# Optimization experiments

Measured on AMD Instinct MI355X. Metric: run time of the kernel, lower is better.

Reference implementation:

```python
import jax, jax.numpy as jnp
import numpy as np

B, T, C = 2, 2048, 2048
H, HD = 16, 128          # n_head, head_dim
DC, DC1 = 672, 672        # kv / q compression dims
DR = 64                   # decoupled rope dim
DN = HD - DR              # nope dim = 64
GATE_CH = 32


def _rope(x, cos, sin):
    # x: (B,T,h,D); cos/sin: (B,T,D//2) -> broadcast over heads
    cos = cos[:, :, None, :]
    sin = sin[:, :, None, :]
    d = x.shape[-1] // 2
    x1, x2 = x[..., :d], x[..., d:]
    return jnp.concatenate([x1 * cos + x2 * sin, -x1 * sin + x2 * cos], axis=-1)


def _rmsnorm(x):
    eps = jnp.finfo(x.dtype).eps
    return x * jax.lax.rsqrt(jnp.mean(jnp.square(x), axis=-1, keepdims=True) + eps)


def setup_inputs() -> dict:
    key = jax.random.key(0)
    ks = jax.random.split(key, 10)
    x = jax.random.normal(ks[0], (B, T, C), jnp.float32)
    ve = jax.random.normal(ks[1], (B, T, H * HD), jnp.float32)
    # rotary tables for d_rope//2 = 32 frequencies
    inv_freq = 1.0 / (10000.0 ** (jnp.arange(DR // 2, dtype=jnp.float32) / (DR // 2)))
    ang = jnp.arange(T, dtype=jnp.float32)[:, None] * inv_freq[None, :]  # (T, DR//2)
    cos = jnp.broadcast_to(jnp.cos(ang)[None], (B, T, DR // 2)).astype(jnp.float32)
    sin = jnp.broadcast_to(jnp.sin(ang)[None], (B, T, DR // 2)).astype(jnp.float32)
    s = 0.02
    w_dkv = s * jax.random.normal(ks[2], (C, DC), jnp.float32)
    w_ukv = s * jax.random.normal(ks[3], (DC, H * (DN + HD)), jnp.float32)
    w_kr = s * jax.random.normal(ks[4], (C, DR), jnp.float32)
    w_dq = s * jax.random.normal(ks[5], (C, DC1), jnp.float32)
    w_q = s * jax.random.normal(ks[6], (DC1, H * HD), jnp.float32)
    w_cproj = s * jax.random.normal(ks[7], (H * HD, C), jnp.float32)
    w_ve_gate = s * jax.random.normal(ks[8], (GATE_CH, H), jnp.float32)
    return {"x": x, "ve": ve, "cos": cos, "sin": sin,
            "w_dkv": w_dkv, "w_ukv": w_ukv, "w_kr": w_kr, "w_dq": w_dq,
            "w_q": w_q, "w_cproj": w_cproj, "w_ve_gate": w_ve_gate,
            "window_size": 0}


def reference(x, ve, cos, sin, w_dkv, w_ukv, w_kr, w_dq, w_q, w_cproj, w_ve_gate, window_size):
    b, t, _ = x.shape
    # low-rank KV path
    c_kv = x @ w_dkv                                   # (B,T,DC)
    kv = (c_kv @ w_ukv).reshape(b, t, H, DN + HD)
    k_nope, v = kv[..., :DN], kv[..., DN:]
    # decoupled rope key (single shared head)
    k_rope = (x @ w_kr).reshape(b, t, 1, DR)
    k_rope = _rope(k_rope, cos, sin)
    # value-embedding gate
    gate = 2.0 * jax.nn.sigmoid(x[..., :GATE_CH] @ w_ve_gate)   # (B,T,H)
    v = v + gate[..., None] * ve.reshape(b, t, H, HD)
    # low-rank Q path
    q = ((x @ w_dq) @ w_q).reshape(b, t, H, HD)
    q_nope, q_rope = q[..., :DN], q[..., DN:]
    q_rope = _rope(q_rope, cos, sin)
    k = jnp.concatenate([k_nope, jnp.broadcast_to(k_rope, (b, t, H, DR))], axis=-1)
    q = jnp.concatenate([q_nope, q_rope], axis=-1)
    q, k = _rmsnorm(q), _rmsnorm(k)
    # causal attention (window_size==0 -> full causal, matching window_size=(-1,-1))
    scale = 1.0 / jnp.sqrt(jnp.float32(HD))
    scores = jnp.einsum('bqhd,bkhd->bhqk', q, k) * scale
    causal = jnp.tril(jnp.ones((t, t), dtype=bool))
    scores = jnp.where(causal[None, None], scores, jnp.finfo(scores.dtype).min)
    att = jax.nn.softmax(scores, axis=-1)
    y = jnp.einsum('bhqk,bkhd->bqhd', att, v).reshape(b, t, H * HD)
    return y @ w_cproj
```

## Files before the change

### kernel.cpp

```cpp
#include <hip/hip_runtime.h>
#include <hip/hip_bf16.h>

typedef unsigned short u16;
typedef unsigned int u32;
typedef __bf16 bf16x8 __attribute__((ext_vector_type(8)));
typedef float f32x4 __attribute__((ext_vector_type(4)));
typedef u16 ushort8 __attribute__((ext_vector_type(8)));

#define TSEQ 2048
#define NHEAD 16

#define GLD16(gp, lp) __builtin_amdgcn_global_load_lds( \
    (__attribute__((address_space(1))) void*)(gp), \
    (__attribute__((address_space(3))) void*)(lp), 16, 0, 0)

static __device__ __forceinline__ float bf2f(u16 u) {
  unsigned int x = ((unsigned int)u) << 16;
  union { unsigned int i; float f; } c; c.i = x; return c.f;
}
static __device__ __forceinline__ u16 f2bf(float f) {
  union { float f; unsigned int i; } c; c.f = f;
  unsigned int x = c.i;
  unsigned int r = (x + 0x7FFFu + ((x >> 16) & 1u)) >> 16;
  return (u16)r;
}
static __device__ __forceinline__ void st_out(u16* p, float v) { *p = f2bf(v); }
static __device__ __forceinline__ void st_out(float* p, float v) { *p = v; }
static __device__ __forceinline__ u32 cvtpk(float lo, float hi) {
  u32 w;
  asm("v_cvt_pk_bf16_f32 %0, %1, %2" : "=v"(w) : "v"(lo), "v"(hi));
  return w;
}

__global__ __launch_bounds__(256) void k_conv_x(const float* __restrict__ x, u16* __restrict__ xb) {
  size_t i = ((size_t)blockIdx.x * 256 + threadIdx.x) * 8;
  float4 a = *(const float4*)(x + i);
  float4 b = *(const float4*)(x + i + 4);
  ushort8 o;
  o[0] = f2bf(a.x); o[1] = f2bf(a.y); o[2] = f2bf(a.z); o[3] = f2bf(a.w);
  o[4] = f2bf(b.x); o[5] = f2bf(b.y); o[6] = f2bf(b.z); o[7] = f2bf(b.w);
  *(ushort8*)(xb + i) = o;
}

__global__ __launch_bounds__(256) void k_tconv_all(const float* __restrict__ w_dkv, const float* __restrict__ w_dq,
                                                   const float* __restrict__ w_kr, const float* __restrict__ w_ukv,
                                                   const float* __restrict__ w_q, const float* __restrict__ w_cp,
                                                   u16* __restrict__ wcatT, u16* __restrict__ wukvT,
                                                   u16* __restrict__ wqT, u16* __restrict__ wcpT) {
  __shared__ float sm[32][33];
  int z = blockIdx.x;
  const float* src; u16* dst; int R, Cc, Rpad, bx, by;
  if (z < 1536)       { src = w_dkv; dst = wcatT;              R = 2048; Cc = 672;  Rpad = 2048; int l = z;        bx = l % 64; by = l / 64; }
  else if (z < 3072)  { src = w_dq;  dst = wcatT + 768 * 2048; R = 2048; Cc = 672;  Rpad = 2048; int l = z - 1536; bx = l % 64; by = l / 64; }
  else if (z < 3200)  { src = w_kr;  dst = wcatT + 1536 * 2048;R = 2048; Cc = 64;   Rpad = 2048; int l = z - 3072; bx = l % 64; by = l / 64; }
  else if (z < 5504)  { src = w_ukv; dst = wukvT;              R = 672;  Cc = 3072; Rpad = 768;  int l = z - 3200; bx = l % 24; by = l / 24; }
  else if (z < 7040)  { src = w_q;   dst = wqT;                R = 672;  Cc = 2048; Rpad = 768;  int l = z - 5504; bx = l % 24; by = l / 24; }
  else                { src = w_cp;  dst = wcpT;               R = 2048; Cc = 2048; Rpad = 2048; int l = z - 7040; bx = l % 64; by = l / 64; }
  int tx = threadIdx.x & 31, ty = threadIdx.x >> 5;
  int r0 = bx * 32, c0 = by * 32;
#pragma unroll
  for (int i = 0; i < 4; i++) {
    int r = r0 + ty + 8 * i;
    int c = c0 + tx;
    sm[ty + 8 * i][tx] = (r < R && c < Cc) ? src[(size_t)r * Cc + c] : 0.f;
  }
  __syncthreads();
#pragma unroll
  for (int i = 0; i < 4; i++) {
    int c = c0 + ty + 8 * i;
    dst[(size_t)c * Rpad + r0 + tx] = f2bf(sm[tx][ty + 8 * i]);
  }
}

__global__ __launch_bounds__(256) void k_gate(const float* __restrict__ x, const float* __restrict__ wg,
                                              float* __restrict__ gate) {
  int idx = blockIdx.x * 256 + threadIdx.x;
  int m = idx >> 4, h = idx & 15;
  const float* xr = x + (size_t)m * 2048;
  float s = 0.f;
#pragma unroll
  for (int j = 0; j < 32; j++) s += xr[j] * wg[j * 16 + h];
  gate[idx] = 2.f / (1.f + __expf(-s));
}

template <typename OT>
__global__ __launch_bounds__(256) void k_gemm128(const u16* __restrict__ A, int lda,
                                                 const u16* __restrict__ BT, int ldb,
                                                 OT* __restrict__ C, int ldc,
                                                 int K) {
  __shared__ __align__(16) u16 As[128 * 32];
  __shared__ __align__(16) u16 Bs[128 * 32];
  int t = threadIdx.x;
  int wid = t >> 6, lane = t & 63;
  int m0 = blockIdx.y * 128, n0 = blockIdx.x * 128;
  int c0 = wid * 2;
  int srow0 = c0 * 16 + (lane >> 2);
  int scol = (lane & 3) * 8;
  const u16* Ag0 = A + (size_t)(m0 + srow0) * lda + scol;
  const u16* Ag1 = A + (size_t)(m0 + srow0 + 16) * lda + scol;
  const u16* Bg0 = BT + (size_t)(n0 + srow0) * ldb + scol;
  const u16* Bg1 = BT + (size_t)(n0 + srow0 + 16) * ldb + scol;
  u16* Al0 = &As[c0 * 512];
  u16* Al1 = &As[c0 * 512 + 512];
  u16* Bl0 = &Bs[c0 * 512];
  u16* Bl1 = &Bs[c0 * 512 + 512];
  int wr = (wid >> 1) * 64, wc = (wid & 1) * 64;
  int fr = lane & 15, fo = (lane >> 4) * 8;
  f32x4 acc[4][4];
#pragma unroll
  for (int m = 0; m < 4; m++)
#pragma unroll
    for (int n = 0; n < 4; n++) acc[m][n] = (f32x4){0, 0, 0, 0};
  for (int k0 = 0; k0 < K; k0 += 32) {
    GLD16(Ag0 + k0, Al0);
    GLD16(Ag1 + k0, Al1);
    GLD16(Bg0 + k0, Bl0);
    GLD16(Bg1 + k0, Bl1);
    __syncthreads();
    bf16x8 af[4], bf[4];
#pragma unroll
    for (int m = 0; m < 4; m++) af[m] = *(const bf16x8*)&As[(wr + m * 16 + fr) * 32 + fo];
#pragma unroll
    for (int n = 0; n < 4; n++) bf[n] = *(const bf16x8*)&Bs[(wc + n * 16 + fr) * 32 + fo];
#pragma unroll
    for (int m = 0; m < 4; m++)
#pragma unroll
      for (int n = 0; n < 4; n++)
        acc[m][n] = __builtin_amdgcn_mfma_f32_16x16x32_bf16(af[m], bf[n], acc[m][n], 0, 0, 0);
    __syncthreads();
  }
  int cr = (lane >> 4) * 4, cc = lane & 15;
#pragma unroll
  for (int m = 0; m < 4; m++)
#pragma unroll
    for (int n = 0; n < 4; n++)
#pragma unroll
      for (int r = 0; r < 4; r++)
        st_out(&C[(size_t)(m0 + wr + m * 16 + cr + r) * ldc + n0 + wc + n * 16 + cc], acc[m][n][r]);
}

__global__ __launch_bounds__(256) void k_gemm_dual(const u16* __restrict__ catout,
                                                   const u16* __restrict__ wukvT,
                                                   u16* __restrict__ kvb,
                                                   const u16* __restrict__ wqT,
                                                   const float* __restrict__ cosp,
                                                   const float* __restrict__ sinp,
                                                   u16* __restrict__ qf) {
  __shared__ __align__(16) u16 As[128 * 32];
  __shared__ __align__(16) u16 Bs[128 * 32];
  int t = threadIdx.x;
  int wid = t >> 6, lane = t & 63;
  int bx = blockIdx.x;
  bool isq = (bx >= 24);
  int nx = isq ? bx - 24 : bx;
  int m0 = blockIdx.y * 128, n0 = nx * 128;
  const u16* A = isq ? catout + 768 : catout;
  const u16* BT = isq ? wqT : wukvT;
  int c0 = wid * 2;
  int srow0 = c0 * 16 + (lane >> 2);
  int scol = (lane & 3) * 8;
  const u16* Ag0 = A + (size_t)(m0 + srow0) * 1664 + scol;
  const u16* Ag1 = A + (size_t)(m0 + srow0 + 16) * 1664 + scol;
  const u16* Bg0 = BT + (size_t)(n0 + srow0) * 768 + scol;
  const u16* Bg1 = BT + (size_t)(n0 + srow0 + 16) * 768 + scol;
  u16* Al0 = &As[c0 * 512];
  u16* Al1 = &As[c0 * 512 + 512];
  u16* Bl0 = &Bs[c0 * 512];
  u16* Bl1 = &Bs[c0 * 512 + 512];
  int wr = (wid >> 1) * 64, wc = (wid & 1) * 64;
  int fr = lane & 15, fo = (lane >> 4) * 8;
  f32x4 acc[4][4];
#pragma unroll
  for (int m = 0; m < 4; m++)
#pragma unroll
    for (int n = 0; n < 4; n++) acc[m][n] = (f32x4){0, 0, 0, 0};
  for (int k0 = 0; k0 < 768; k0 += 32) {
    GLD16(Ag0 + k0, Al0);
    GLD16(Ag1 + k0, Al1);
    GLD16(Bg0 + k0, Bl0);
    GLD16(Bg1 + k0, Bl1);
    __syncthreads();
    bf16x8 af[4], bf[4];
#pragma unroll
    for (int m = 0; m < 4; m++) af[m] = *(const bf16x8*)&As[(wr + m * 16 + fr) * 32 + fo];
#pragma unroll
    for (int n = 0; n < 4; n++) bf[n] = *(const bf16x8*)&Bs[(wc + n * 16 + fr) * 32 + fo];
#pragma unroll
    for (int m = 0; m < 4; m++)
#pragma unroll
      for (int n = 0; n < 4; n++)
        acc[m][n] = __builtin_amdgcn_mfma_f32_16x16x32_bf16(af[m], bf[n], acc[m][n], 0, 0, 0);
    __syncthreads();
  }
  int cr = (lane >> 4) * 4, cc = lane & 15;
  if (!isq) {
#pragma unroll
    for (int m = 0; m < 4; m++)
#pragma unroll
      for (int n = 0; n < 4; n++)
#pragma unroll
        for (int r = 0; r < 4; r++)
          kvb[(size_t)(m0 + wr + m * 16 + cr + r) * 3072 + n0 + wc + n * 16 + cc] = f2bf(acc[m][n][r]);
    return;
  }
  int h = nx;
  int wch = wid & 1;
  int wrg = wid >> 1;
  if (wch == 1) {
#pragma unroll
    for (int m = 0; m < 4; m++)
#pragma unroll
      for (int r = 0; r < 4; r++) {
        int grow = m0 + wr + m * 16 + cr + r;
#pragma unroll
        for (int n = 0; n < 2; n++) {
          int i = n * 16 + cc;
          float cth = cosp[(size_t)grow * 32 + i];
          float sth = sinp[(size_t)grow * 32 + i];
          float x1 = acc[m][n][r], x2 = acc[m][n + 2][r];
          acc[m][n][r]     = x1 * cth + x2 * sth;
          acc[m][n + 2][r] = x2 * cth - x1 * sth;
        }
      }
  }
  float part[4][4];
#pragma unroll
  for (int m = 0; m < 4; m++)
#pragma unroll
    for (int r = 0; r < 4; r++) {
      float s2 = 0.f;
#pragma unroll
      for (int n = 0; n < 4; n++) s2 += acc[m][n][r] * acc[m][n][r];
#pragma unroll
      for (int o = 1; o < 16; o <<= 1) s2 += __shfl_xor(s2, o, 64);
      part[m][r] = s2;
    }
  float* xs = (float*)As;
  if (cc == 0) {
#pragma unroll
    for (int m = 0; m < 4; m++)
#pragma unroll
      for (int r = 0; r < 4; r++)
        xs[(wrg * 2 + wch) * 64 + m * 16 + cr + r] = part[m][r];
  }
  __syncthreads();
#pragma unroll
  for (int m = 0; m < 4; m++)
#pragma unroll
    for (int r = 0; r < 4; r++) {
      int lrow = m * 16 + cr + r;
      float tot = part[m][r] + xs[(wrg * 2 + (wch ^ 1)) * 64 + lrow];
      float rms = rsqrtf(tot * (1.f / 128.f) + 1.1920929e-7f) * 0.1275174245f;
      int grow = m0 + wr + lrow;
      int b2 = grow >> 11, tt = grow & 2047;
      size_t base = (((size_t)(b2 * NHEAD + h)) * TSEQ + tt) * 128 + wch * 64;
#pragma unroll
      for (int n = 0; n < 4; n++)
        qf[base + n * 16 + cc] = f2bf(acc[m][n][r] * rms);
    }
}

__global__ __launch_bounds__(256) void k_build_k(const u16* __restrict__ kv, const u16* __restrict__ kr,
                                                 const float* __restrict__ cosp, const float* __restrict__ sinp,
                                                 u16* __restrict__ ksw) {
  __shared__ __align__(16) u16 sm[8192];
  int tid = threadIdx.x, wid = tid >> 6, lane = tid & 63;
  int bh = blockIdx.x >> 5, tile = blockIdx.x & 31;
  int b = bh >> 4, h = bh & 15;
  int d0 = lane * 2;
  for (int rr = 0; rr < 16; rr++) {
    int row = wid * 16 + rr;
    int t = tile * 64 + row;
    int m = b * TSEQ + t;
    float v[2];
#pragma unroll
    for (int e = 0; e < 2; e++) {
      int d = d0 + e;
      float val;
      if (d < 64) {
        val = bf2f(kv[(size_t)m * 3072 + h * 192 + d]);
      } else {
        int dd = d - 64, i = dd & 31;
        float c = cosp[m * 32 + i], s = sinp[m * 32 + i];
        float x1 = bf2f(kr[(size_t)m * 1664 + i]), x2 = bf2f(kr[(size_t)m * 1664 + 32 + i]);
        val = (dd < 32) ? (x1 * c + x2 * s) : (x2 * c - x1 * s);
      }
      v[e] = val;
    }
    float ss = v[0] * v[0] + v[1] * v[1];
#pragma unroll
    for (int o = 1; o < 64; o <<= 1) ss += __shfl_xor(ss, o, 64);
    float rms = rsqrtf(ss * (1.f / 128.f) + 1.1920929e-7f);
    int a = (row * 256 + d0 * 2) ^ ((row & 7) << 4);
    sm[a >> 1] = f2bf(v[0] * rms);
    sm[(a >> 1) + 1] = f2bf(v[1] * rms);
  }
  __syncthreads();
  u16* dst = ksw + ((size_t)(bh * 32 + tile)) * 8192 + tid * 32;
  const u16* src = sm + tid * 32;
#pragma unroll
  for (int j = 0; j < 4; j++)
    *(ushort8*)(dst + j * 8) = *(const ushort8*)(src + j * 8);
}

__global__ __launch_bounds__(256) void k_build_v(const u16* __restrict__ kv, const float* __restrict__ ve,
                                                 const float* __restrict__ gate, u16* __restrict__ vsw) {
  __shared__ __align__(16) char sm[128 * 128];
  int bh = blockIdx.x >> 5, tile = blockIdx.x & 31;
  int t0 = tile * 64;
  int b = bh >> 4, h = bh & 15;
  int tt = threadIdx.x >> 2, dp = (threadIdx.x & 3) * 32;
  int m = b * TSEQ + t0 + tt;
  float g = gate[m * 16 + h];
  const u16* kvp = kv + (size_t)m * 3072 + h * 192 + 64 + dp;
  const float* vep = ve + (size_t)m * 2048 + h * 128 + dp;
  ushort8 kvv[4];
  float4 vev[8];
#pragma unroll
  for (int u = 0; u < 4; u++) kvv[u] = *(const ushort8*)(kvp + u * 8);
#pragma unroll
  for (int u = 0; u < 8; u++) vev[u] = *(const float4*)(vep + u * 4);
#pragma unroll
  for (int j = 0; j < 32; j++) {
    float vvf = ((const float*)&vev[j >> 2])[j & 3];
    float v = bf2f(kvv[j >> 3][j & 7]) + g * vvf;
    int row = dp + j;
    int a = row * 128 + tt * 2;
    *(u16*)(sm + (a ^ ((row & 7) << 4))) = f2bf(v);
  }
  __syncthreads();
  u16* dst = vsw + ((size_t)(bh * 32 + tile)) * 8192 + threadIdx.x * 32;
  const u16* src = (const u16*)sm + threadIdx.x * 32;
#pragma unroll
  for (int j = 0; j < 4; j++)
    *(ushort8*)(dst + j * 8) = *(const ushort8*)(src + j * 8);
}

__global__ __launch_bounds__(256, 2) void k_attn(const u16* __restrict__ qf, const u16* __restrict__ ksw,
                                                 const u16* __restrict__ vsw, u16* __restrict__ y) {
  __shared__ __align__(16) u16 kvbuf[2][2][8192];
  __shared__ __align__(16) char plds_all[4][4096];
  int tid = threadIdx.x, wid = tid >> 6, lane = tid & 63;
  int gq = lane >> 4, c = lane & 15;
  int task = (blockIdx.x & 7) * 64 + (blockIdx.x >> 3);
  int bh = task >> 4;
  int tq = task & 15;
  int qb = ((task >> 5) & 1) ? tq : 15 - tq;
  int nt = 2 * qb + 2;
  int q0w = qb * 128 + wid * 32;
  const u16* qp = qf + (size_t)bh * TSEQ * 128;
  const u16* kswb = ksw + (size_t)bh * 32 * 8192;
  const u16* vswb = vsw + (size_t)bh * 32 * 8192;
  char* plds = plds_all[wid];
  int swz = (c & 7) << 4;
  bf16x8 qfr[2][4];
#pragma unroll
  for (int rg = 0; rg < 2; rg++)
#pragma unroll
    for (int kc = 0; kc < 4; kc++)
      qfr[rg][kc] = *(const bf16x8*)(qp + (size_t)(q0w + rg * 16 + c) * 128 + kc * 32 + gq * 8);
  f32x4 oacc[2][8];
#pragma unroll
  for (int rg = 0; rg < 2; rg++)
#pragma unroll
    for (int nd = 0; nd < 8; nd++) oacc[rg][nd] = (f32x4){0, 0, 0, 0};
  float mreg[2] = {-1e30f, -1e30f}, lreg[2] = {0.f, 0.f};
  int chunk = wid * 4;
#pragma unroll
  for (int j = 0; j < 4; j++) {
    GLD16(kswb + (chunk + j) * 512 + lane * 8, &kvbuf[0][0][(chunk + j) * 512]);
    GLD16(vswb + (chunk + j) * 512 + lane * 8, &kvbuf[0][1][(chunk + j) * 512]);
  }
  __syncthreads();
  for (int it = 0; it < nt; it++) {
    int cur = it & 1;
    if (it + 1 < nt) {
      const u16* kt = kswb + (size_t)(it + 1) * 8192;
      const u16* vt = vswb + (size_t)(it + 1) * 8192;
#pragma unroll
      for (int j = 0; j < 4; j++) {
        GLD16(kt + (chunk + j) * 512 + lane * 8, &kvbuf[cur ^ 1][0][(chunk + j) * 512]);
        GLD16(vt + (chunk + j) * 512 + lane * 8, &kvbuf[cur ^ 1][1][(chunk + j) * 512]);
      }
    }
    int kt0 = it * 64;
    if (kt0 <= q0w + 31) {
      const char* Kt = (const char*)kvbuf[cur][0];
      const char* Vt = (const char*)kvbuf[cur][1];
      bool maskit = (kt0 + 63 > q0w);
      f32x4 sacc[2][4];
#pragma unroll
      for (int rg = 0; rg < 2; rg++)
#pragma unroll
        for (int s = 0; s < 4; s++) sacc[rg][s] = (f32x4){0, 0, 0, 0};
#pragma unroll
      for (int s = 0; s < 4; s++) {
        int row = s * 16 + c;
#pragma unroll
        for (int kc = 0; kc < 4; kc++) {
          int a = (row * 256 + (kc * 32 + gq * 8) * 2) ^ ((row & 7) << 4);
          bf16x8 kfr = *(const bf16x8*)(Kt + a);
          sacc[0][s] = __builtin_amdgcn_mfma_f32_16x16x32_bf16(kfr, qfr[0][kc], sacc[0][s], 0, 0, 0);
          sacc[1][s] = __builtin_amdgcn_mfma_f32_16x16x32_bf16(kfr, qfr[1][kc], sacc[1][s], 0, 0, 0);
        }
      }
      if (maskit) {
#pragma unroll
        for (int rg = 0; rg < 2; rg++) {
          int qrow = q0w + rg * 16 + c;
#pragma unroll
          for (int s = 0; s < 4; s++)
#pragma unroll
            for (int r = 0; r < 4; r++) {
              int key = kt0 + s * 16 + gq * 4 + r;
              sacc[rg][s][r] = (key <= qrow) ? sacc[rg][s][r] : -3e38f;
            }
        }
      }
      float mx[2];
#pragma unroll
      for (int rg = 0; rg < 2; rg++) {
        float m2 = sacc[rg][0][0];
#pragma unroll
        for (int s = 0; s < 4; s++)
#pragma unroll
          for (int r = 0; r < 4; r++) m2 = fmaxf(m2, sacc[rg][s][r]);
        m2 = fmaxf(m2, __shfl_xor(m2, 16, 64));
        m2 = fmaxf(m2, __shfl_xor(m2, 32, 64));
        mx[rg] = m2;
      }
      bool ok = (mx[0] - mreg[0] <= 11.f) && (mx[1] - mreg[1] <= 11.f);
      if (!__all(ok)) {
#pragma unroll
        for (int rg = 0; rg < 2; rg++) {
          float mn = fmaxf(mreg[rg], mx[rg]);
          float fac = exp2f(mreg[rg] - mn);
          lreg[rg] *= fac;
          float fq[4];
#pragma unroll
          for (int r = 0; r < 4; r++) fq[r] = __shfl(fac, gq * 4 + r, 64);
#pragma unroll
          for (int nd = 0; nd < 8; nd++)
#pragma unroll
            for (int r = 0; r < 4; r++) oacc[rg][nd][r] *= fq[r];
          mreg[rg] = mn;
        }
      }
#pragma unroll
      for (int rg = 0; rg < 2; rg++) {
        float p[4][4];
        float rs = 0.f;
#pragma unroll
        for (int s = 0; s < 4; s++)
#pragma unroll
          for (int r = 0; r < 4; r++) {
            p[s][r] = exp2f(sacc[rg][s][r] - mreg[rg]);
            rs += p[s][r];
          }
        rs += __shfl_xor(rs, 16, 64);
        rs += __shfl_xor(rs, 32, 64);
        lreg[rg] += rs;
#pragma unroll
        for (int s = 0; s < 4; s++) {
          u32 w0 = cvtpk(p[s][0], p[s][1]);
          u32 w1 = cvtpk(p[s][2], p[s][3]);
          int a = (rg * 2048 + c * 128 + s * 32 + gq * 8) ^ swz;
          *(uint2*)(plds + a) = make_uint2(w0, w1);
        }
      }
#pragma unroll
      for (int kc2 = 0; kc2 < 2; kc2++) {
        int a0 = (c * 128 + kc2 * 64 + gq * 16) ^ swz;
        bf16x8 pa0 = *(const bf16x8*)(plds + a0);
        bf16x8 pa1 = *(const bf16x8*)(plds + 2048 + a0);
#pragma unroll
        for (int nd = 0; nd < 8; nd++) {
          int vrow = nd * 16 + c;
          int av = (vrow * 128 + (kc2 * 32 + gq * 8) * 2) ^ ((vrow & 7) << 4);
          bf16x8 vfr = *(const bf16x8*)(Vt + av);
          oacc[0][nd] = __builtin_amdgcn_mfma_f32_16x16x32_bf16(pa0, vfr, oacc[0][nd], 0, 0, 0);
          oacc[1][nd] = __builtin_amdgcn_mfma_f32_16x16x32_bf16(pa1, vfr, oacc[1][nd], 0, 0, 0);
        }
      }
    }
    __syncthreads();
  }
  int b2 = bh >> 4, h2 = bh & 15;
#pragma unroll
  for (int rg = 0; rg < 2; rg++) {
    float linv = 1.f / lreg[rg];
    float inv[4];
#pragma unroll
    for (int r = 0; r < 4; r++) inv[r] = __shfl(linv, gq * 4 + r, 64);
#pragma unroll
    for (int nd = 0; nd < 8; nd++) {
#pragma unroll
      for (int r = 0; r < 4; r++) {
        size_t offo = ((size_t)(b2 * TSEQ + q0w + rg * 16 + gq * 4 + r)) * 2048 + h2 * 128 + nd * 16 + c;
        y[offo] = f2bf(oacc[rg][nd][r] * inv[r]);
      }
    }
  }
}

extern "C" void kernel_launch(void* const* d_in, const int* in_sizes, int n_in,
                              void* d_out, int out_size, void* d_ws, size_t ws_size,
                              hipStream_t stream) {
  (void)in_sizes; (void)n_in; (void)out_size; (void)ws_size;
  const float* x      = (const float*)d_in[0];
  const float* ve     = (const float*)d_in[1];
  const float* cosp   = (const float*)d_in[2];
  const float* sinp   = (const float*)d_in[3];
  const float* w_dkv  = (const float*)d_in[4];
  const float* w_ukv  = (const float*)d_in[5];
  const float* w_kr   = (const float*)d_in[6];
  const float* w_dq   = (const float*)d_in[7];
  const float* w_q    = (const float*)d_in[8];
  const float* w_cp   = (const float*)d_in[9];
  const float* w_vg   = (const float*)d_in[10];
  float* out = (float*)d_out;

  char* ws = (char*)d_ws;
  size_t off = 0;
  auto alloc = [&](size_t bytes) -> char* {
    char* p = ws + off;
    off += (bytes + 255) & ~(size_t)255;
    return p;
  };
  u16* xb     = (u16*)alloc(4096ull * 2048 * 2);
  u16* wcatT  = (u16*)alloc(1664ull * 2048 * 2);
  u16* wukvT  = (u16*)alloc(3072ull * 768 * 2);
  u16* wqT    = (u16*)alloc(2048ull * 768 * 2);
  u16* wcpT   = (u16*)alloc(2048ull * 2048 * 2);
  u16* catout = (u16*)alloc(4096ull * 1664 * 2);
  u16* kvb    = (u16*)alloc(4096ull * 3072 * 2);
  float* gateb = (float*)alloc(4096ull * 16 * 4);
  u16* qfb    = (u16*)alloc(2ull * 16 * 2048 * 128 * 2);
  u16* kswb   = (u16*)alloc(32ull * 32 * 8192 * 2);
  u16* vswb   = (u16*)alloc(32ull * 32 * 8192 * 2);
  u16* yb = xb;

  k_conv_x<<<dim3(4096), dim3(256), 0, stream>>>(x, xb);
  k_tconv_all<<<dim3(11136), dim3(256), 0, stream>>>(w_dkv, w_dq, w_kr, w_ukv, w_q, w_cp,
                                                     wcatT, wukvT, wqT, wcpT);
  k_gate<<<dim3(256), dim3(256), 0, stream>>>(x, w_vg, gateb);

  k_gemm128<u16><<<dim3(13, 32), dim3(256), 0, stream>>>(xb, 2048, wcatT, 2048, catout, 1664, 2048);
  k_gemm_dual<<<dim3(40, 32), dim3(256), 0, stream>>>(catout, wukvT, kvb, wqT, cosp, sinp, qfb);

  k_build_k<<<dim3(1024), dim3(256), 0, stream>>>(kvb, catout + 1536, cosp, sinp, kswb);
  k_build_v<<<dim3(1024), dim3(256), 0, stream>>>(kvb, ve, gateb, vswb);

  k_attn<<<dim3(512), dim3(256), 0, stream>>>(qfb, kswb, vswb, yb);

  k_gemm128<float><<<dim3(16, 32), dim3(256), 0, stream>>>(yb, 2048, wcpT, 2048, out, 2048, 2048);
}
```

Measured before the change: 329.9 us.

## Split long causal attention query blocks across two workgroups with merge kernel

Query blocks 8-15, which have the longest causal KV ranges, are now split into two halves of the KV loop, each run by its own workgroup, raising the grid from 512 to 768 blocks. The partial O, m and l values are written to scratch space that reuses the catout buffer, and a new merge kernel combines them with a log-sum-exp rescale. The aim is to even out per-block work and shorten the tail of the causal attention launch, at the cost of extra fp32 partial traffic and one more kernel launch.

```diff
diff --git a/kernel.cpp b/kernel.cpp
--- a/kernel.cpp
+++ b/kernel.cpp
@@ -337,16 +337,30 @@
 }
 
 __global__ __launch_bounds__(256, 2) void k_attn(const u16* __restrict__ qf, const u16* __restrict__ ksw,
-                                                 const u16* __restrict__ vsw, u16* __restrict__ y) {
+                                                 const u16* __restrict__ vsw, u16* __restrict__ y,
+                                                 float* __restrict__ opart, float* __restrict__ mpart,
+                                                 float* __restrict__ lpart) {
   __shared__ __align__(16) u16 kvbuf[2][2][8192];
   __shared__ __align__(16) char plds_all[4][4096];
   int tid = threadIdx.x, wid = tid >> 6, lane = tid & 63;
   int gq = lane >> 4, c = lane & 15;
-  int task = (blockIdx.x & 7) * 64 + (blockIdx.x >> 3);
-  int bh = task >> 4;
-  int tq = task & 15;
-  int qb = ((task >> 5) & 1) ? tq : 15 - tq;
-  int nt = 2 * qb + 2;
+  int xcd = blockIdx.x & 7, r0r = blockIdx.x >> 3;
+  int bh, qb, it0, it1, pidx = -1;
+  if (r0r < 64) {
+    bh = xcd * 4 + (r0r & 3);
+    int sub = r0r >> 2;
+    qb = 15 - (sub >> 1);
+    int half = sub & 1;
+    it0 = half ? (qb + 1) : 0;
+    it1 = half ? (2 * qb + 2) : (qb + 1);
+    pidx = bh * 16 + (qb - 8) * 2 + half;
+  } else {
+    int rr = r0r - 64;
+    bh = xcd * 4 + (rr & 3);
+    qb = 7 - (rr >> 2);
+    it0 = 0;
+    it1 = 2 * qb + 2;
+  }
   int q0w = qb * 128 + wid * 32;
   const u16* qp = qf + (size_t)bh * TSEQ * 128;
   const u16* kswb = ksw + (size_t)bh * 32 * 8192;
@@ -368,13 +382,13 @@
   int chunk = wid * 4;
 #pragma unroll
   for (int j = 0; j < 4; j++) {
-    GLD16(kswb + (chunk + j) * 512 + lane * 8, &kvbuf[0][0][(chunk + j) * 512]);
-    GLD16(vswb + (chunk + j) * 512 + lane * 8, &kvbuf[0][1][(chunk + j) * 512]);
+    GLD16(kswb + (size_t)it0 * 8192 + (chunk + j) * 512 + lane * 8, &kvbuf[0][0][(chunk + j) * 512]);
+    GLD16(vswb + (size_t)it0 * 8192 + (chunk + j) * 512 + lane * 8, &kvbuf[0][1][(chunk + j) * 512]);
   }
   __syncthreads();
-  for (int it = 0; it < nt; it++) {
-    int cur = it & 1;
-    if (it + 1 < nt) {
+  for (int it = it0; it < it1; it++) {
+    int cur = (it - it0) & 1;
+    if (it + 1 < it1) {
       const u16* kt = kswb + (size_t)(it + 1) * 8192;
       const u16* vt = vswb + (size_t)(it + 1) * 8192;
 #pragma unroll
@@ -485,6 +499,22 @@
     }
     __syncthreads();
   }
+  if (pidx >= 0) {
+    float* op = opart + (size_t)pidx * 16384;
+#pragma unroll
+    for (int rg = 0; rg < 2; rg++) {
+#pragma unroll
+      for (int nd = 0; nd < 8; nd++)
+#pragma unroll
+        for (int r = 0; r < 4; r++)
+          op[(wid * 32 + rg * 16 + gq * 4 + r) * 128 + nd * 16 + c] = oacc[rg][nd][r];
+      if (gq == 0) {
+        mpart[pidx * 128 + wid * 32 + rg * 16 + c] = mreg[rg];
+        lpart[pidx * 128 + wid * 32 + rg * 16 + c] = lreg[rg];
+      }
+    }
+    return;
+  }
   int b2 = bh >> 4, h2 = bh & 15;
 #pragma unroll
   for (int rg = 0; rg < 2; rg++) {
@@ -500,6 +530,24 @@
         y[offo] = f2bf(oacc[rg][nd][r] * inv[r]);
       }
     }
+  }
+}
+
+__global__ __launch_bounds__(256) void k_merge(const float* __restrict__ opart, const float* __restrict__ mpart,
+                                               const float* __restrict__ lpart, u16* __restrict__ y) {
+  int blk = blockIdx.x;
+  int bh = blk >> 3, qb = 8 + (blk & 7);
+  int p0 = bh * 16 + (qb - 8) * 2, p1 = p0 + 1;
+  int b2 = bh >> 4, h2 = bh & 15;
+  for (int e = threadIdx.x; e < 16384; e += 256) {
+    int row = e >> 7, col = e & 127;
+    float m0 = mpart[p0 * 128 + row], m1 = mpart[p1 * 128 + row];
+    float mm = fmaxf(m0, m1);
+    float e0 = exp2f(m0 - mm), e1 = exp2f(m1 - mm);
+    float l = lpart[p0 * 128 + row] * e0 + lpart[p1 * 128 + row] * e1;
+    float o = opart[(size_t)p0 * 16384 + row * 128 + col] * e0 +
+              opart[(size_t)p1 * 16384 + row * 128 + col] * e1;
+    y[((size_t)(b2 * TSEQ + qb * 128 + row)) * 2048 + h2 * 128 + col] = f2bf(o / l);
   }
 }
 
@@ -539,6 +587,9 @@
   u16* kswb   = (u16*)alloc(32ull * 32 * 8192 * 2);
   u16* vswb   = (u16*)alloc(32ull * 32 * 8192 * 2);
   u16* yb = xb;
+  float* opart = (float*)catout;
+  float* mpart = opart + 512 * 16384;
+  float* lpart = mpart + 512 * 128;
 
   k_conv_x<<<dim3(4096), dim3(256), 0, stream>>>(x, xb);
   k_tconv_all<<<dim3(11136), dim3(256), 0, stream>>>(w_dkv, w_dq, w_kr, w_ukv, w_q, w_cp,
@@ -551,7 +602,8 @@
   k_build_k<<<dim3(1024), dim3(256), 0, stream>>>(kvb, catout + 1536, cosp, sinp, kswb);
   k_build_v<<<dim3(1024), dim3(256), 0, stream>>>(kvb, ve, gateb, vswb);
 
-  k_attn<<<dim3(512), dim3(256), 0, stream>>>(qfb, kswb, vswb, yb);
+  k_attn<<<dim3(768), dim3(256), 0, stream>>>(qfb, kswb, vswb, yb, opart, mpart, lpart);
+  k_merge<<<dim3(256), dim3(256), 0, stream>>>(opart, mpart, lpart, yb);
 
   k_gemm128<float><<<dim3(16, 32), dim3(256), 0, stream>>>(yb, 2048, wcpT, 2048, out, 2048, 2048);
 }
```

After: 346.1 us. +4.9%, slower.
